# Optimization experiments

Measured on AMD Instinct MI355X. Metric: run time of the kernel, lower is better.

Reference implementation:

```python
import jax, jax.numpy as jnp
import numpy as np

N_NODES = 8192
IN_DIM = 128
HIDDEN = 128
N_EDGES = 262144


def gcn_layer(x, W, b, src, dst, n):
    # GCNConv: h = D^{-1/2}(A+I)D^{-1/2} (x @ W) + b, with added self-loops
    h = x @ W  # [n, out]
    loop = jnp.arange(n, dtype=src.dtype)
    s = jnp.concatenate([src, loop])
    d = jnp.concatenate([dst, loop])
    deg = jax.ops.segment_sum(jnp.ones_like(s, dtype=h.dtype), d, num_segments=n)
    dinv = jax.lax.rsqrt(deg)  # deg >= 1 due to self-loops
    norm = dinv[s] * dinv[d]  # [E+n]
    msg = h[s] * norm[:, None]
    out = jax.ops.segment_sum(msg, d, num_segments=n)
    return out + b


def setup_inputs() -> dict:
    key = jax.random.key(0)
    ks = jax.random.split(key, 10)
    g = 1.0 / np.sqrt(HIDDEN)
    inp = {
        "x": jax.random.normal(ks[0], (N_NODES, IN_DIM), dtype=jnp.float32),
        "edge_index": jax.random.randint(ks[1], (2, N_EDGES), 0, N_NODES, dtype=jnp.int32),
        "W1": jax.random.normal(ks[2], (IN_DIM, HIDDEN), dtype=jnp.float32) * (1.0 / np.sqrt(IN_DIM)),
        "b1": jnp.zeros((HIDDEN,), dtype=jnp.float32),
        "W2": jax.random.normal(ks[3], (HIDDEN, HIDDEN), dtype=jnp.float32) * g,
        "b2": jnp.zeros((HIDDEN,), dtype=jnp.float32),
        "W_out": jax.random.normal(ks[4], (HIDDEN, HIDDEN), dtype=jnp.float32) * g,
        "b_out": jnp.zeros((HIDDEN,), dtype=jnp.float32),
        "W_edge": jax.random.normal(ks[5], (2 * HIDDEN,), dtype=jnp.float32) * (1.0 / np.sqrt(2 * HIDDEN)),
        "b_edge": jnp.zeros((), dtype=jnp.float32),
    }
    return inp


def reference(x, edge_index, W1, b1, W2, b2, W_out, b_out, W_edge, b_edge):
    src, dst = edge_index[0], edge_index[1]
    n = x.shape[0]
    h = jax.nn.relu(gcn_layer(x, W1, b1, src, dst, n))
    h = jax.nn.relu(gcn_layer(h, W2, b2, src, dst, n))
    h = h @ W_out + b_out  # [n, hidden]
    # edge_proj(cat(x_i, x_j)) decomposes: logits[i,j] = h_i.w_i + h_j.w_j + b
    w_i, w_j = W_edge[:HIDDEN], W_edge[HIDDEN:]
    a = h @ w_i  # [n]
    c = h @ w_j  # [n]
    edge_logits = a[:, None] + c[None, :] + b_edge  # [n, n]
    return edge_logits
```

## Files before the change

kernel.cpp:

```cpp
#include <hip/hip_runtime.h>

#define NN 8192
#define NE 262144
#define DIM 128
#define BCAP 128

typedef float f32x4 __attribute__((ext_vector_type(4)));
typedef float f32x2 __attribute__((ext_vector_type(2)));

__device__ __forceinline__ float4 f4fma(float s, float4 w, float4 acc) {
    acc.x = fmaf(s, w.x, acc.x);
    acc.y = fmaf(s, w.y, acc.y);
    acc.z = fmaf(s, w.z, acc.z);
    acc.w = fmaf(s, w.w, acc.w);
    return acc;
}
__device__ __forceinline__ float f4dot(float4 a, float4 b) {
    return fmaf(a.x, b.x, fmaf(a.y, b.y, fmaf(a.z, b.z, a.w * b.w)));
}

__global__ __launch_bounds__(256) void zero_kernel(int* __restrict__ cnt) {
    cnt[blockIdx.x * 256 + threadIdx.x] = 0;
}

__global__ __launch_bounds__(256) void scatter_uv(const int* __restrict__ src,
                                                  const int* __restrict__ dst,
                                                  int* __restrict__ cnt,
                                                  int* __restrict__ bucket,
                                                  const float* __restrict__ Wout,
                                                  const float* __restrict__ bout,
                                                  const float* __restrict__ we,
                                                  const float* __restrict__ bedge,
                                                  float* __restrict__ u,
                                                  float* __restrict__ v,
                                                  float* __restrict__ beta) {
    int k = threadIdx.x;
    if (blockIdx.x < 1024) {
        int e = blockIdx.x * 256 + k;
        int d = dst[e];
        int p = atomicAdd(&cnt[d], 1);
        if (p < BCAP) bucket[(d << 7) + p] = src[e];
        return;
    }
    if (k < DIM) {
        const float4* W4 = (const float4*)(Wout + (k << 7));
        const float4* we4 = (const float4*)we;
        float su = 0.f, sv = 0.f;
#pragma unroll
        for (int j = 0; j < 32; ++j) {
            float4 w = W4[j];
            su += f4dot(w, we4[j]);
            sv += f4dot(w, we4[32 + j]);
        }
        u[k] = su;
        v[k] = sv;
    }
    __shared__ float red[256];
    red[k] = (k < DIM) ? bout[k] * we[k] : 0.f;
    __syncthreads();
    for (int off = 128; off >= 1; off >>= 1) {
        if (k < off) red[k] += red[k + off];
        __syncthreads();
    }
    float b0 = red[0];
    __syncthreads();
    red[k] = (k < DIM) ? bout[k] * we[DIM + k] : 0.f;
    __syncthreads();
    for (int off = 128; off >= 1; off >>= 1) {
        if (k < off) red[k] += red[k + off];
        __syncthreads();
    }
    if (k == 0) {
        beta[0] = b0 + bedge[0];
        beta[1] = red[0];
    }
}

__global__ __launch_bounds__(256) void gemm_pre(const float* __restrict__ X,
                                                const float* __restrict__ W,
                                                const int* __restrict__ cnt,
                                                f32x4* __restrict__ G) {
    __shared__ float4 Wl[128 * 32];
    __shared__ float4 Xl[32 * 32];
    int tid = threadIdx.x;
    int rbase = blockIdx.x * 32;

    const float4* W4 = (const float4*)W;
#pragma unroll
    for (int i = 0; i < 16; ++i) Wl[i * 256 + tid] = W4[i * 256 + tid];
    const float4* X4 = (const float4*)(X + rbase * DIM);
#pragma unroll
    for (int i = 0; i < 4; ++i) Xl[i * 256 + tid] = X4[i * 256 + tid];
    __syncthreads();

    int tx = tid & 31;
    int ty = tid >> 5;
    float4 acc[4];
#pragma unroll
    for (int i = 0; i < 4; ++i) acc[i] = make_float4(0.f, 0.f, 0.f, 0.f);

    for (int k4 = 0; k4 < 32; ++k4) {
        float4 w0 = Wl[(k4 * 4 + 0) * 32 + tx];
        float4 w1 = Wl[(k4 * 4 + 1) * 32 + tx];
        float4 w2 = Wl[(k4 * 4 + 2) * 32 + tx];
        float4 w3 = Wl[(k4 * 4 + 3) * 32 + tx];
#pragma unroll
        for (int i = 0; i < 4; ++i) {
            float4 xv = Xl[(ty * 4 + i) * 32 + k4];
            acc[i] = f4fma(xv.x, w0, acc[i]);
            acc[i] = f4fma(xv.y, w1, acc[i]);
            acc[i] = f4fma(xv.z, w2, acc[i]);
            acc[i] = f4fma(xv.w, w3, acc[i]);
        }
    }

#pragma unroll
    for (int i = 0; i < 4; ++i) {
        int r = rbase + ty * 4 + i;
        float dv = rsqrtf((float)(cnt[r] + 1));
        f32x4 o = {acc[i].x * dv, acc[i].y * dv, acc[i].z * dv, acc[i].w * dv};
        __builtin_nontemporal_store(o, G + r * 32 + tx);
    }
}

__global__ __launch_bounds__(256) void gather_scale(const float* __restrict__ G1,
                                                    const int* __restrict__ cnt,
                                                    const int* __restrict__ bucket,
                                                    const float* __restrict__ b1,
                                                    f32x2* __restrict__ S2) {
    int node = blockIdx.x * 4 + (threadIdx.x >> 6);
    int lane = threadIdx.x & 63;
    const float2* G12 = (const float2*)G1;

    int deg = cnt[node];
    float dv = rsqrtf((float)(deg + 1));
    int i0 = __builtin_nontemporal_load(bucket + (node << 7) + lane);
    int i1 = __builtin_nontemporal_load(bucket + (node << 7) + 64 + lane);

    float2 p0 = G12[node * 64 + lane];
    float2 p1 = {0.f, 0.f}, p2 = {0.f, 0.f}, p3 = {0.f, 0.f};

    int d4 = deg & ~3;
    for (int e = 0; e < d4; e += 4) {
        int s0 = __shfl((e + 0) >= 64 ? i1 : i0, (e + 0) & 63);
        int s1 = __shfl((e + 1) >= 64 ? i1 : i0, (e + 1) & 63);
        int s2 = __shfl((e + 2) >= 64 ? i1 : i0, (e + 2) & 63);
        int s3 = __shfl((e + 3) >= 64 ? i1 : i0, (e + 3) & 63);
        float2 t0 = G12[s0 * 64 + lane];
        float2 t1 = G12[s1 * 64 + lane];
        float2 t2 = G12[s2 * 64 + lane];
        float2 t3 = G12[s3 * 64 + lane];
        p0.x += t0.x; p0.y += t0.y;
        p1.x += t1.x; p1.y += t1.y;
        p2.x += t2.x; p2.y += t2.y;
        p3.x += t3.x; p3.y += t3.y;
    }
    for (int e = d4; e < deg; ++e) {
        int s = __shfl(e >= 64 ? i1 : i0, e & 63);
        float2 t = G12[s * 64 + lane];
        p0.x += t.x; p0.y += t.y;
    }
    float yx = (p0.x + p1.x) + (p2.x + p3.x);
    float yy = (p0.y + p1.y) + (p2.y + p3.y);

    const float2* B2 = (const float2*)b1;
    float2 bb = B2[lane];
    f32x2 o;
    o.x = fmaxf(fmaf(yx, dv, bb.x), 0.f) * dv;
    o.y = fmaxf(fmaf(yy, dv, bb.y), 0.f) * dv;
    __builtin_nontemporal_store(o, S2 + node * 64 + lane);
}

__global__ __launch_bounds__(256) void gemm_mid(const float* __restrict__ X,
                                                const float* __restrict__ W,
                                                f32x4* __restrict__ G) {
    __shared__ float4 Wl[128 * 32];
    __shared__ float4 Xl[32 * 32];
    int tid = threadIdx.x;
    int rbase = blockIdx.x * 32;

    const float4* W4 = (const float4*)W;
#pragma unroll
    for (int i = 0; i < 16; ++i) Wl[i * 256 + tid] = W4[i * 256 + tid];
    const float4* X4 = (const float4*)(X + rbase * DIM);
#pragma unroll
    for (int i = 0; i < 4; ++i) Xl[i * 256 + tid] = X4[i * 256 + tid];
    __syncthreads();

    int tx = tid & 31;
    int ty = tid >> 5;
    float4 acc[4];
#pragma unroll
    for (int i = 0; i < 4; ++i) acc[i] = make_float4(0.f, 0.f, 0.f, 0.f);

    for (int k4 = 0; k4 < 32; ++k4) {
        float4 w0 = Wl[(k4 * 4 + 0) * 32 + tx];
        float4 w1 = Wl[(k4 * 4 + 1) * 32 + tx];
        float4 w2 = Wl[(k4 * 4 + 2) * 32 + tx];
        float4 w3 = Wl[(k4 * 4 + 3) * 32 + tx];
#pragma unroll
        for (int i = 0; i < 4; ++i) {
            float4 xv = Xl[(ty * 4 + i) * 32 + k4];
            acc[i] = f4fma(xv.x, w0, acc[i]);
            acc[i] = f4fma(xv.y, w1, acc[i]);
            acc[i] = f4fma(xv.z, w2, acc[i]);
            acc[i] = f4fma(xv.w, w3, acc[i]);
        }
    }

#pragma unroll
    for (int i = 0; i < 4; ++i) {
        int r = rbase + ty * 4 + i;
        f32x4 o = {acc[i].x, acc[i].y, acc[i].z, acc[i].w};
        __builtin_nontemporal_store(o, G + r * 32 + tx);
    }
}

__global__ __launch_bounds__(256) void agg_head(const float* __restrict__ G2,
                                                const int* __restrict__ cnt,
                                                const int* __restrict__ bucket,
                                                const float* __restrict__ b2,
                                                const float* __restrict__ u,
                                                const float* __restrict__ v,
                                                const float* __restrict__ beta,
                                                float* __restrict__ a,
                                                float* __restrict__ c) {
    int node = blockIdx.x * 4 + (threadIdx.x >> 6);
    int lane = threadIdx.x & 63;
    const float2* G22 = (const float2*)G2;

    int deg = cnt[node];
    float dv = rsqrtf((float)(deg + 1));
    int i0 = __builtin_nontemporal_load(bucket + (node << 7) + lane);
    int i1 = __builtin_nontemporal_load(bucket + (node << 7) + 64 + lane);

    float2 p0 = G22[node * 64 + lane];
    float2 p1 = {0.f, 0.f}, p2 = {0.f, 0.f}, p3 = {0.f, 0.f};

    int d4 = deg & ~3;
    for (int e = 0; e < d4; e += 4) {
        int s0 = __shfl((e + 0) >= 64 ? i1 : i0, (e + 0) & 63);
        int s1 = __shfl((e + 1) >= 64 ? i1 : i0, (e + 1) & 63);
        int s2 = __shfl((e + 2) >= 64 ? i1 : i0, (e + 2) & 63);
        int s3 = __shfl((e + 3) >= 64 ? i1 : i0, (e + 3) & 63);
        float2 t0 = G22[s0 * 64 + lane];
        float2 t1 = G22[s1 * 64 + lane];
        float2 t2 = G22[s2 * 64 + lane];
        float2 t3 = G22[s3 * 64 + lane];
        p0.x += t0.x; p0.y += t0.y;
        p1.x += t1.x; p1.y += t1.y;
        p2.x += t2.x; p2.y += t2.y;
        p3.x += t3.x; p3.y += t3.y;
    }
    for (int e = d4; e < deg; ++e) {
        int s = __shfl(e >= 64 ? i1 : i0, e & 63);
        float2 t = G22[s * 64 + lane];
        p0.x += t.x; p0.y += t.y;
    }
    float yx = (p0.x + p1.x) + (p2.x + p3.x);
    float yy = (p0.y + p1.y) + (p2.y + p3.y);

    const float2* B2 = (const float2*)b2;
    float2 bb = B2[lane];
    float h0 = fmaxf(fmaf(yx, dv, bb.x), 0.f);
    float h1 = fmaxf(fmaf(yy, dv, bb.y), 0.f);

    float2 uu = ((const float2*)u)[lane];
    float2 vv = ((const float2*)v)[lane];
    float pa = h0 * uu.x + h1 * uu.y;
    float pc = h0 * vv.x + h1 * vv.y;
#pragma unroll
    for (int off = 32; off >= 1; off >>= 1) {
        pa += __shfl_xor(pa, off);
        pc += __shfl_xor(pc, off);
    }
    if (lane == 0) {
        a[node] = pa + beta[0];
        c[node] = pc + beta[1];
    }
}

__global__ __launch_bounds__(256) void out_kernel(const float* __restrict__ a,
                                                  const float* __restrict__ c,
                                                  f32x4* __restrict__ out) {
    const f32x4* c4 = (const f32x4*)c;
    size_t base = (size_t)blockIdx.x * 1024 + threadIdx.x;
#pragma unroll
    for (int q = 0; q < 4; ++q) {
        size_t idx = base + q * 256;
        int i = (int)(idx >> 11);
        int j4 = (int)(idx & 2047);
        f32x4 r = c4[j4] + a[i];
        out[idx] = r;
    }
}

extern "C" void kernel_launch(void* const* d_in, const int* in_sizes, int n_in,
                              void* d_out, int out_size, void* d_ws, size_t ws_size,
                              hipStream_t stream) {
    const float* x    = (const float*)d_in[0];
    const int*   ei   = (const int*)d_in[1];
    const float* W1   = (const float*)d_in[2];
    const float* b1   = (const float*)d_in[3];
    const float* W2   = (const float*)d_in[4];
    const float* b2   = (const float*)d_in[5];
    const float* Wout = (const float*)d_in[6];
    const float* bout = (const float*)d_in[7];
    const float* We   = (const float*)d_in[8];
    const float* bedge= (const float*)d_in[9];
    const int* src = ei;
    const int* dst = ei + NE;

    int* cnt     = (int*)d_ws;
    int* bucket  = cnt + NN;
    float* u     = (float*)(bucket + NN * BCAP);
    float* v     = u + DIM;
    float* beta  = v + DIM;
    float* g1    = beta + 16;
    float* s2    = g1 + NN * DIM;
    float* g2    = s2 + NN * DIM;
    float* av    = g2 + NN * DIM;
    float* cv    = av + NN;

    float* out = (float*)d_out;

    zero_kernel<<<32, 256, 0, stream>>>(cnt);
    scatter_uv<<<1025, 256, 0, stream>>>(src, dst, cnt, bucket,
                                         Wout, bout, We, bedge, u, v, beta);
    gemm_pre<<<NN / 32, 256, 0, stream>>>(x, W1, cnt, (f32x4*)g1);
    gather_scale<<<NN / 4, 256, 0, stream>>>(g1, cnt, bucket, b1, (f32x2*)s2);
    gemm_mid<<<NN / 32, 256, 0, stream>>>(s2, W2, (f32x4*)g2);
    agg_head<<<NN / 4, 256, 0, stream>>>(g2, cnt, bucket, b2, u, v, beta, av, cv);
    out_kernel<<<(NN * NN / 4) / 1024, 256, 0, stream>>>(av, cv, (f32x4*)out);
}
```

Before: 110.5 us.

## Fuse first GEMM with edge bucketing and move source-degree scaling into gather

The first X@W1 GEMM no longer depends on degree counts, so it is merged into one launch with the edge scatter and head-vector precompute, with blocks split by index. This removes one kernel launch and lets the dense GEMM overlap with the atomic bucketing. The per-source rsqrt(deg) scaling moves into the first gather loop, which adds a cnt load per edge. Both gather loops are unrolled to 8 independent accumulators and clamp the degree to the bucket capacity.

```diff
diff --git a/kernel.cpp b/kernel.cpp
--- a/kernel.cpp
+++ b/kernel.cpp
@@ -23,39 +23,85 @@
     cnt[blockIdx.x * 256 + threadIdx.x] = 0;
 }
 
-__global__ __launch_bounds__(256) void scatter_uv(const int* __restrict__ src,
-                                                  const int* __restrict__ dst,
-                                                  int* __restrict__ cnt,
-                                                  int* __restrict__ bucket,
-                                                  const float* __restrict__ Wout,
-                                                  const float* __restrict__ bout,
-                                                  const float* __restrict__ we,
-                                                  const float* __restrict__ bedge,
-                                                  float* __restrict__ u,
-                                                  float* __restrict__ v,
-                                                  float* __restrict__ beta) {
-    int k = threadIdx.x;
-    if (blockIdx.x < 1024) {
-        int e = blockIdx.x * 256 + k;
+__global__ __launch_bounds__(256) void fused_pre(const float* __restrict__ X,
+                                                 const float* __restrict__ W,
+                                                 f32x4* __restrict__ G,
+                                                 const int* __restrict__ src,
+                                                 const int* __restrict__ dst,
+                                                 int* __restrict__ cnt,
+                                                 int* __restrict__ bucket,
+                                                 const float* __restrict__ Wout,
+                                                 const float* __restrict__ bout,
+                                                 const float* __restrict__ we,
+                                                 const float* __restrict__ bedge,
+                                                 float* __restrict__ u,
+                                                 float* __restrict__ v,
+                                                 float* __restrict__ beta) {
+    __shared__ float4 Wl[128 * 32];
+    __shared__ float4 Xl[32 * 32];
+    int tid = threadIdx.x;
+    int bid = blockIdx.x;
+
+    if (bid < 256) {
+        int rbase = bid * 32;
+        const float4* W4 = (const float4*)W;
+#pragma unroll
+        for (int i = 0; i < 16; ++i) Wl[i * 256 + tid] = W4[i * 256 + tid];
+        const float4* X4 = (const float4*)(X + rbase * DIM);
+#pragma unroll
+        for (int i = 0; i < 4; ++i) Xl[i * 256 + tid] = X4[i * 256 + tid];
+        __syncthreads();
+
+        int tx = tid & 31;
+        int ty = tid >> 5;
+        float4 acc[4];
+#pragma unroll
+        for (int i = 0; i < 4; ++i) acc[i] = make_float4(0.f, 0.f, 0.f, 0.f);
+
+        for (int k4 = 0; k4 < 32; ++k4) {
+            float4 w0 = Wl[(k4 * 4 + 0) * 32 + tx];
+            float4 w1 = Wl[(k4 * 4 + 1) * 32 + tx];
+            float4 w2 = Wl[(k4 * 4 + 2) * 32 + tx];
+            float4 w3 = Wl[(k4 * 4 + 3) * 32 + tx];
+#pragma unroll
+            for (int i = 0; i < 4; ++i) {
+                float4 xv = Xl[(ty * 4 + i) * 32 + k4];
+                acc[i] = f4fma(xv.x, w0, acc[i]);
+                acc[i] = f4fma(xv.y, w1, acc[i]);
+                acc[i] = f4fma(xv.z, w2, acc[i]);
+                acc[i] = f4fma(xv.w, w3, acc[i]);
+            }
+        }
+#pragma unroll
+        for (int i = 0; i < 4; ++i) {
+            int r = rbase + ty * 4 + i;
+            f32x4 o = {acc[i].x, acc[i].y, acc[i].z, acc[i].w};
+            __builtin_nontemporal_store(o, G + r * 32 + tx);
+        }
+        return;
+    }
+    if (bid < 1280) {
+        int e = (bid - 256) * 256 + tid;
         int d = dst[e];
         int p = atomicAdd(&cnt[d], 1);
         if (p < BCAP) bucket[(d << 7) + p] = src[e];
         return;
     }
+    float* red = (float*)Xl;
+    int k = tid;
     if (k < DIM) {
-        const float4* W4 = (const float4*)(Wout + (k << 7));
+        const float4* W4o = (const float4*)(Wout + (k << 7));
         const float4* we4 = (const float4*)we;
         float su = 0.f, sv = 0.f;
 #pragma unroll
         for (int j = 0; j < 32; ++j) {
-            float4 w = W4[j];
+            float4 w = W4o[j];
             su += f4dot(w, we4[j]);
             sv += f4dot(w, we4[32 + j]);
         }
         u[k] = su;
         v[k] = sv;
     }
-    __shared__ float red[256];
     red[k] = (k < DIM) ? bout[k] * we[k] : 0.f;
     __syncthreads();
     for (int off = 128; off >= 1; off >>= 1) {
@@ -73,53 +119,6 @@
     if (k == 0) {
         beta[0] = b0 + bedge[0];
         beta[1] = red[0];
-    }
-}
-
-__global__ __launch_bounds__(256) void gemm_pre(const float* __restrict__ X,
-                                                const float* __restrict__ W,
-                                                const int* __restrict__ cnt,
-                                                f32x4* __restrict__ G) {
-    __shared__ float4 Wl[128 * 32];
-    __shared__ float4 Xl[32 * 32];
-    int tid = threadIdx.x;
-    int rbase = blockIdx.x * 32;
-
-    const float4* W4 = (const float4*)W;
-#pragma unroll
-    for (int i = 0; i < 16; ++i) Wl[i * 256 + tid] = W4[i * 256 + tid];
-    const float4* X4 = (const float4*)(X + rbase * DIM);
-#pragma unroll
-    for (int i = 0; i < 4; ++i) Xl[i * 256 + tid] = X4[i * 256 + tid];
-    __syncthreads();
-
-    int tx = tid & 31;
-    int ty = tid >> 5;
-    float4 acc[4];
-#pragma unroll
-    for (int i = 0; i < 4; ++i) acc[i] = make_float4(0.f, 0.f, 0.f, 0.f);
-
-    for (int k4 = 0; k4 < 32; ++k4) {
-        float4 w0 = Wl[(k4 * 4 + 0) * 32 + tx];
-        float4 w1 = Wl[(k4 * 4 + 1) * 32 + tx];
-        float4 w2 = Wl[(k4 * 4 + 2) * 32 + tx];
-        float4 w3 = Wl[(k4 * 4 + 3) * 32 + tx];
-#pragma unroll
-        for (int i = 0; i < 4; ++i) {
-            float4 xv = Xl[(ty * 4 + i) * 32 + k4];
-            acc[i] = f4fma(xv.x, w0, acc[i]);
-            acc[i] = f4fma(xv.y, w1, acc[i]);
-            acc[i] = f4fma(xv.z, w2, acc[i]);
-            acc[i] = f4fma(xv.w, w3, acc[i]);
-        }
-    }
-
-#pragma unroll
-    for (int i = 0; i < 4; ++i) {
-        int r = rbase + ty * 4 + i;
-        float dv = rsqrtf((float)(cnt[r] + 1));
-        f32x4 o = {acc[i].x * dv, acc[i].y * dv, acc[i].z * dv, acc[i].w * dv};
-        __builtin_nontemporal_store(o, G + r * 32 + tx);
     }
 }
 
@@ -132,36 +131,42 @@
     int lane = threadIdx.x & 63;
     const float2* G12 = (const float2*)G1;
 
-    int deg = cnt[node];
-    float dv = rsqrtf((float)(deg + 1));
+    int degree = cnt[node];
+    float dv = rsqrtf((float)(degree + 1));
+    int deg = min(degree, BCAP);
     int i0 = __builtin_nontemporal_load(bucket + (node << 7) + lane);
     int i1 = __builtin_nontemporal_load(bucket + (node << 7) + 64 + lane);
 
-    float2 p0 = G12[node * 64 + lane];
-    float2 p1 = {0.f, 0.f}, p2 = {0.f, 0.f}, p3 = {0.f, 0.f};
-
-    int d4 = deg & ~3;
-    for (int e = 0; e < d4; e += 4) {
-        int s0 = __shfl((e + 0) >= 64 ? i1 : i0, (e + 0) & 63);
-        int s1 = __shfl((e + 1) >= 64 ? i1 : i0, (e + 1) & 63);
-        int s2 = __shfl((e + 2) >= 64 ? i1 : i0, (e + 2) & 63);
-        int s3 = __shfl((e + 3) >= 64 ? i1 : i0, (e + 3) & 63);
-        float2 t0 = G12[s0 * 64 + lane];
-        float2 t1 = G12[s1 * 64 + lane];
-        float2 t2 = G12[s2 * 64 + lane];
-        float2 t3 = G12[s3 * 64 + lane];
-        p0.x += t0.x; p0.y += t0.y;
-        p1.x += t1.x; p1.y += t1.y;
-        p2.x += t2.x; p2.y += t2.y;
-        p3.x += t3.x; p3.y += t3.y;
-    }
-    for (int e = d4; e < deg; ++e) {
+    float2 selfv = G12[node * 64 + lane];
+    float ax = selfv.x * dv, ay = selfv.y * dv;
+    float px[8], py[8];
+#pragma unroll
+    for (int k = 0; k < 8; ++k) { px[k] = 0.f; py[k] = 0.f; }
+
+    int d8 = deg & ~7;
+    for (int e = 0; e < d8; e += 8) {
+        int s[8];
+#pragma unroll
+        for (int k = 0; k < 8; ++k) s[k] = __shfl((e + k) >= 64 ? i1 : i0, (e + k) & 63);
+#pragma unroll
+        for (int k = 0; k < 8; ++k) {
+            int ck = cnt[s[k]];
+            float2 t = G12[s[k] * 64 + lane];
+            float w = rsqrtf((float)(ck + 1));
+            px[k] = fmaf(t.x, w, px[k]);
+            py[k] = fmaf(t.y, w, py[k]);
+        }
+    }
+    for (int e = d8; e < deg; ++e) {
         int s = __shfl(e >= 64 ? i1 : i0, e & 63);
+        int ck = cnt[s];
         float2 t = G12[s * 64 + lane];
-        p0.x += t.x; p0.y += t.y;
-    }
-    float yx = (p0.x + p1.x) + (p2.x + p3.x);
-    float yy = (p0.y + p1.y) + (p2.y + p3.y);
+        float w = rsqrtf((float)(ck + 1));
+        ax = fmaf(t.x, w, ax);
+        ay = fmaf(t.y, w, ay);
+    }
+    float yx = ax + ((px[0] + px[1]) + (px[2] + px[3])) + ((px[4] + px[5]) + (px[6] + px[7]));
+    float yy = ay + ((py[0] + py[1]) + (py[2] + py[3])) + ((py[4] + py[5]) + (py[6] + py[7]));
 
     const float2* B2 = (const float2*)b1;
     float2 bb = B2[lane];
@@ -229,36 +234,38 @@
     int lane = threadIdx.x & 63;
     const float2* G22 = (const float2*)G2;
 
-    int deg = cnt[node];
-    float dv = rsqrtf((float)(deg + 1));
+    int degree = cnt[node];
+    float dv = rsqrtf((float)(degree + 1));
+    int deg = min(degree, BCAP);
     int i0 = __builtin_nontemporal_load(bucket + (node << 7) + lane);
     int i1 = __builtin_nontemporal_load(bucket + (node << 7) + 64 + lane);
 
-    float2 p0 = G22[node * 64 + lane];
-    float2 p1 = {0.f, 0.f}, p2 = {0.f, 0.f}, p3 = {0.f, 0.f};
-
-    int d4 = deg & ~3;
-    for (int e = 0; e < d4; e += 4) {
-        int s0 = __shfl((e + 0) >= 64 ? i1 : i0, (e + 0) & 63);
-        int s1 = __shfl((e + 1) >= 64 ? i1 : i0, (e + 1) & 63);
-        int s2 = __shfl((e + 2) >= 64 ? i1 : i0, (e + 2) & 63);
-        int s3 = __shfl((e + 3) >= 64 ? i1 : i0, (e + 3) & 63);
-        float2 t0 = G22[s0 * 64 + lane];
-        float2 t1 = G22[s1 * 64 + lane];
-        float2 t2 = G22[s2 * 64 + lane];
-        float2 t3 = G22[s3 * 64 + lane];
-        p0.x += t0.x; p0.y += t0.y;
-        p1.x += t1.x; p1.y += t1.y;
-        p2.x += t2.x; p2.y += t2.y;
-        p3.x += t3.x; p3.y += t3.y;
-    }
-    for (int e = d4; e < deg; ++e) {
+    float2 selfv = G22[node * 64 + lane];
+    float ax = selfv.x, ay = selfv.y;
+    float px[8], py[8];
+#pragma unroll
+    for (int k = 0; k < 8; ++k) { px[k] = 0.f; py[k] = 0.f; }
+
+    int d8 = deg & ~7;
+    for (int e = 0; e < d8; e += 8) {
+        int s[8];
+#pragma unroll
+        for (int k = 0; k < 8; ++k) s[k] = __shfl((e + k) >= 64 ? i1 : i0, (e + k) & 63);
+#pragma unroll
+        for (int k = 0; k < 8; ++k) {
+            float2 t = G22[s[k] * 64 + lane];
+            px[k] += t.x;
+            py[k] += t.y;
+        }
+    }
+    for (int e = d8; e < deg; ++e) {
         int s = __shfl(e >= 64 ? i1 : i0, e & 63);
         float2 t = G22[s * 64 + lane];
-        p0.x += t.x; p0.y += t.y;
-    }
-    float yx = (p0.x + p1.x) + (p2.x + p3.x);
-    float yy = (p0.y + p1.y) + (p2.y + p3.y);
+        ax += t.x;
+        ay += t.y;
+    }
+    float yx = ax + ((px[0] + px[1]) + (px[2] + px[3])) + ((px[4] + px[5]) + (px[6] + px[7]));
+    float yy = ay + ((py[0] + py[1]) + (py[2] + py[3])) + ((py[4] + py[5]) + (py[6] + py[7]));
 
     const float2* B2 = (const float2*)b2;
     float2 bb = B2[lane];
@@ -325,9 +332,8 @@
     float* out = (float*)d_out;
 
     zero_kernel<<<32, 256, 0, stream>>>(cnt);
-    scatter_uv<<<1025, 256, 0, stream>>>(src, dst, cnt, bucket,
-                                         Wout, bout, We, bedge, u, v, beta);
-    gemm_pre<<<NN / 32, 256, 0, stream>>>(x, W1, cnt, (f32x4*)g1);
+    fused_pre<<<1281, 256, 0, stream>>>(x, W1, (f32x4*)g1, src, dst, cnt, bucket,
+                                        Wout, bout, We, bedge, u, v, beta);
     gather_scale<<<NN / 4, 256, 0, stream>>>(g1, cnt, bucket, b1, (f32x2*)s2);
     gemm_mid<<<NN / 32, 256, 0, stream>>>(s2, W2, (f32x4*)g2);
     agg_head<<<NN / 4, 256, 0, stream>>>(g2, cnt, bucket, b2, u, v, beta, av, cv);
```

After: 110.0 us. No clear change (-0.5%).
